# Performance work log

Hardware: AMD Instinct MI355X
Metric: run time of the kernel (lower is better)

## Reference

```python
import jax, jax.numpy as jnp
import numpy as np
from jax import lax

BS, T, D = 32, 2048, 256
H, L = 256, 2

def setup_inputs() -> dict:
    key = jax.random.key(0)
    ks = jax.random.split(key, 5)
    s = 1.0 / np.sqrt(H)
    x = jax.random.normal(ks[0], (BS, T, D), dtype=jnp.float32)
    Wx = jax.random.uniform(ks[1], (L, 3 * H, D), jnp.float32, -s, s)
    Wh = jax.random.uniform(ks[2], (L, 3 * H, H), jnp.float32, -s, s)
    bx = jax.random.uniform(ks[3], (L, 3 * H), jnp.float32, -s, s)
    bh = jax.random.uniform(ks[4], (L, 3 * H), jnp.float32, -s, s)
    return {"x": x, "Wx": Wx, "Wh": Wh, "bx": bx, "bh": bh}

def _gru_scan(gx, Wh, bh, h0):
    # gx: (T, bs, L, 3H) precomputed input-side gates; h0: (bs, L, H)
    def step(h, gx_t):
        gh = jnp.einsum('blh,lgh->blg', h, Wh) + bh  # (bs, L, 3H)
        xr, xz, xn = jnp.split(gx_t, 3, axis=-1)
        hr, hz, hn = jnp.split(gh, 3, axis=-1)
        r = jax.nn.sigmoid(xr + hr)
        z = jax.nn.sigmoid(xz + hz)
        n = jnp.tanh(xn + r * hn)
        h_new = (1.0 - z) * n + z * h
        return h_new, h_new
    _, hs = lax.scan(step, h0, gx)  # (T, bs, L, H)
    return hs

def reference(x, Wx, Wh, bx, bh):
    bs, t, _ = x.shape
    l, h = Wh.shape[0], Wh.shape[2]
    # Input-side gate projections for all timesteps/layers at once (each layer
    # consumes the raw input x_t, as in the source module).
    gx = jnp.einsum('btd,lgd->tblg', x, Wx) + bx  # (T, bs, L, 3H)
    h0 = jnp.zeros((bs, l, h), x.dtype)
    fwd = _gru_scan(gx, Wh, bh, h0)               # (T, bs, L, H)
    bwd = _gru_scan(gx[::-1], Wh, bh, h0)[::-1]   # reversed-time pass, same weights
    out = jnp.concatenate([fwd, bwd], axis=-1)    # (T, bs, L, 2H)
    # ordering matches source: for t in range(T): for layer in range(L)
    out = out.transpose(1, 0, 2, 3).reshape(bs, t * l, 2 * h)
    return out
```

## Files before the change

kernel.cpp:

```cpp
#include <hip/hip_runtime.h>


typedef _Float16 half8 __attribute__((ext_vector_type(8)));
typedef _Float16 half2_t __attribute__((ext_vector_type(2)));
typedef float floatx4 __attribute__((ext_vector_type(4)));

__device__ __forceinline__ float sigmoidf_fast(float x) {
    return 1.0f / (1.0f + __expf(-x));
}

__device__ __forceinline__ float tanh_fast(float x) {
    float ax = fabsf(x);
    float e = __expf(-2.0f * ax);
    float t = (1.0f - e) / (1.0f + e);
    return copysignf(t, x);
}

__global__ __launch_bounds__(256) void gemm_gx_kernel(
    const float* __restrict__ x,
    const float* __restrict__ Wx,
    const float* __restrict__ bx,
    _Float16* __restrict__ gx)
{
    __shared__ __align__(16) char lds[32768];
    _Float16* As = (_Float16*)lds;
    _Float16* Bs = (_Float16*)(lds + 8192);

    const int tid = threadIdx.x;
    const int m0 = blockIdx.x * 128;
    const int n0 = blockIdx.y * 128;
    const int wave = tid >> 6;
    const int lane = tid & 63;
    const int wm = wave & 1;
    const int wn = wave >> 1;
    const int frag = lane & 15;
    const int kg = lane >> 4;

    floatx4 acc[4][4];
#pragma unroll
    for (int a = 0; a < 4; ++a)
#pragma unroll
        for (int b = 0; b < 4; ++b)
            acc[a][b] = (floatx4){0.f, 0.f, 0.f, 0.f};

    for (int k0 = 0; k0 < 256; k0 += 32) {
        __syncthreads();
#pragma unroll
        for (int rep = 0; rep < 2; ++rep) {
            int idx = tid + rep * 256;
            int row = idx >> 2;
            int kc = idx & 3;
            const float4* ap = (const float4*)(x + (size_t)(m0 + row) * 256 + k0 + kc * 8);
            const float4* bp = (const float4*)(Wx + (size_t)(n0 + row) * 256 + k0 + kc * 8);
            float4 a0 = ap[0], a1 = ap[1];
            float4 b0 = bp[0], b1 = bp[1];
            half8 av = {(_Float16)a0.x, (_Float16)a0.y, (_Float16)a0.z, (_Float16)a0.w,
                        (_Float16)a1.x, (_Float16)a1.y, (_Float16)a1.z, (_Float16)a1.w};
            half8 bv = {(_Float16)b0.x, (_Float16)b0.y, (_Float16)b0.z, (_Float16)b0.w,
                        (_Float16)b1.x, (_Float16)b1.y, (_Float16)b1.z, (_Float16)b1.w};
            *(half8*)(As + (kc * 128 + row) * 8) = av;
            *(half8*)(Bs + (kc * 128 + row) * 8) = bv;
        }
        __syncthreads();

        half8 af[4], bfr[4];
#pragma unroll
        for (int tm = 0; tm < 4; ++tm)
            af[tm] = *(const half8*)(As + (kg * 128 + wm * 64 + tm * 16 + frag) * 8);
#pragma unroll
        for (int tn = 0; tn < 4; ++tn)
            bfr[tn] = *(const half8*)(Bs + (kg * 128 + wn * 64 + tn * 16 + frag) * 8);
#pragma unroll
        for (int tm = 0; tm < 4; ++tm)
#pragma unroll
            for (int tn = 0; tn < 4; ++tn)
                acc[tm][tn] = __builtin_amdgcn_mfma_f32_16x16x32_f16(
                    af[tm], bfr[tn], acc[tm][tn], 0, 0, 0);
    }

    __syncthreads();
    _Float16* epi = (_Float16*)lds;
#pragma unroll
    for (int tm = 0; tm < 4; ++tm) {
#pragma unroll
        for (int tn = 0; tn < 4; ++tn) {
            int col = wn * 64 + tn * 16 + frag;
            float bias = bx[n0 + col];
#pragma unroll
            for (int r = 0; r < 4; ++r) {
                int rowc = wm * 64 + tm * 16 + kg * 4 + r;
                epi[rowc * 128 + col] = (_Float16)(acc[tm][tn][r] + bias);
            }
        }
    }
    __syncthreads();

    int row = tid >> 1;
    int hs = tid & 1;
    int gm = m0 + row;
    int bb = gm >> 11;
    int tt = gm & 2047;
    int l = n0 / 768;
    int g0 = n0 - l * 768 + hs * 64;
    size_t oidx = (((size_t)bb * 2 + l) * 2048 + tt) * 768 + g0;
    const uint4* s = (const uint4*)(epi + row * 128 + hs * 64);
    uint4* d = (uint4*)(gx + oidx);
#pragma unroll
    for (int j = 0; j < 8; ++j) d[j] = s[j];
}

__global__ __launch_bounds__(512)
__attribute__((amdgpu_waves_per_eu(2, 2)))
void gru_scan_kernel(
    const float* __restrict__ Wh,
    const float* __restrict__ bh,
    const _Float16* __restrict__ gx,
    float* __restrict__ out)
{
    const int c = blockIdx.x;
    const int b = c & 31;
    const int l = (c >> 5) & 1;
    const int dir = c >> 6;
    const int tid = threadIdx.x;
    const int wave = tid >> 6;
    const int lane = tid & 63;
    const int q = lane >> 5;
    const int i = wave * 32 + (lane & 31);

    __shared__ __align__(16) _Float16 h2[2][256];

    half2_t wr[64], wz[64], wn_[64];
    {
        const float2* pr = (const float2*)(Wh + ((size_t)l * 768 + i) * 256 + q * 128);
        const float2* pz = (const float2*)(Wh + ((size_t)l * 768 + 256 + i) * 256 + q * 128);
        const float2* pn = (const float2*)(Wh + ((size_t)l * 768 + 512 + i) * 256 + q * 128);
#pragma unroll
        for (int j = 0; j < 64; ++j) {
            float2 a = pr[j], bb2 = pz[j], cc = pn[j];
            wr[j]  = (half2_t){(_Float16)a.x, (_Float16)a.y};
            wz[j]  = (half2_t){(_Float16)bb2.x, (_Float16)bb2.y};
            wn_[j] = (half2_t){(_Float16)cc.x, (_Float16)cc.y};
        }
    }

    const float bhr = bh[l * 768 + i];
    const float bhz = bh[l * 768 + 256 + i];
    const float bhn = bh[l * 768 + 512 + i];

    const _Float16* gxp = gx + (size_t)(b * 2 + l) * 2048 * 768;
    float* outp = out + (size_t)b * 2048 * 1024 + (size_t)l * 512 + dir * 256 + i;

    if (tid < 256) h2[0][tid] = (_Float16)0.f;

    const int t0 = dir ? 2047 : 0;
    _Float16 cxr = gxp[(size_t)t0 * 768 + i];
    _Float16 cxz = gxp[(size_t)t0 * 768 + 256 + i];
    _Float16 cxn = gxp[(size_t)t0 * 768 + 512 + i];
    __syncthreads();

    float hreg = 0.f;

    for (int s = 0; s < 2048; ++s) {
        const int t = dir ? (2047 - s) : s;
        const int sn = (s < 2047) ? (s + 1) : s;
        const int tn = dir ? (2047 - sn) : sn;

        _Float16 pxr = gxp[(size_t)tn * 768 + i];
        _Float16 pxz = gxp[(size_t)tn * 768 + 256 + i];
        _Float16 pxn = gxp[(size_t)tn * 768 + 512 + i];

        float ar = 0.f, az = 0.f, an = 0.f;
        const uint4* hbase = (const uint4*)(&h2[s & 1][0]) + (q << 4);
#pragma unroll
        for (int j = 0; j < 16; ++j) {
            uint4 hv = hbase[j];
            half2_t h0 = __builtin_bit_cast(half2_t, hv.x);
            half2_t h1 = __builtin_bit_cast(half2_t, hv.y);
            half2_t hg = __builtin_bit_cast(half2_t, hv.z);
            half2_t h3 = __builtin_bit_cast(half2_t, hv.w);
            ar = __builtin_amdgcn_fdot2(wr[4 * j + 0], h0, ar, false);
            az = __builtin_amdgcn_fdot2(wz[4 * j + 0], h0, az, false);
            an = __builtin_amdgcn_fdot2(wn_[4 * j + 0], h0, an, false);
            ar = __builtin_amdgcn_fdot2(wr[4 * j + 1], h1, ar, false);
            az = __builtin_amdgcn_fdot2(wz[4 * j + 1], h1, az, false);
            an = __builtin_amdgcn_fdot2(wn_[4 * j + 1], h1, an, false);
            ar = __builtin_amdgcn_fdot2(wr[4 * j + 2], hg, ar, false);
            az = __builtin_amdgcn_fdot2(wz[4 * j + 2], hg, az, false);
            an = __builtin_amdgcn_fdot2(wn_[4 * j + 2], hg, an, false);
            ar = __builtin_amdgcn_fdot2(wr[4 * j + 3], h3, ar, false);
            az = __builtin_amdgcn_fdot2(wz[4 * j + 3], h3, az, false);
            an = __builtin_amdgcn_fdot2(wn_[4 * j + 3], h3, an, false);
        }

        ar += __shfl_xor(ar, 32, 64);
        az += __shfl_xor(az, 32, 64);
        an += __shfl_xor(an, 32, 64);

        float r = sigmoidf_fast((float)cxr + ar + bhr);
        float z = sigmoidf_fast((float)cxz + az + bhz);
        float n = tanh_fast((float)cxn + an + r * (an * 0.f + (az * 0.f) + (ar * 0.f) + bhn + an - an + (float)0) + 0.f * an);
        (void)n;
        float ghn = an + bhn;
        n = tanh_fast((float)cxn + r * ghn);
        float hnew = (1.f - z) * n + z * hreg;
        hreg = hnew;

        if (q == 0) {
            outp[(size_t)t * 1024] = hnew;
            h2[(s + 1) & 1][i] = (_Float16)hnew;
        }
        cxr = pxr; cxz = pxz; cxn = pxn;
        __syncthreads();
    }
}

extern "C" void kernel_launch(void* const* d_in, const int* in_sizes, int n_in,
                              void* d_out, int out_size, void* d_ws, size_t ws_size,
                              hipStream_t stream) {
    const float* x  = (const float*)d_in[0];
    const float* Wx = (const float*)d_in[1];
    const float* Wh = (const float*)d_in[2];
    const float* bx = (const float*)d_in[3];
    const float* bh = (const float*)d_in[4];
    float* out = (float*)d_out;
    _Float16* gxbuf = (_Float16*)d_ws;

    gemm_gx_kernel<<<dim3(512, 12), 256, 0, stream>>>(x, Wx, bx, gxbuf);

    gru_scan_kernel<<<dim3(128), 512, 0, stream>>>(Wh, bh, gxbuf, out);
}
```

Before: 2.881 ms.

## Split GRU scan dot products across four lanes per unit with 1024 threads

The recurrent scan kernel now uses 1024 threads per block, so each hidden unit's 256-long dot product is split across four lane groups of 64 elements instead of two of 128. This halves per-thread weight registers and per-step serial FMA work, at the cost of an extra cross-lane shuffle reduction and a wider block barrier each step. The LDS reads of h are rotated per lane group to avoid bank conflicts, the dead redundant tanh computation is removed, and gx values are converted to float when loaded.

```diff
diff --git a/kernel.cpp b/kernel.cpp
--- a/kernel.cpp
+++ b/kernel.cpp
@@ -109,9 +109,7 @@
     for (int j = 0; j < 8; ++j) d[j] = s[j];
 }
 
-__global__ __launch_bounds__(512)
-__attribute__((amdgpu_waves_per_eu(2, 2)))
-void gru_scan_kernel(
+__global__ __launch_bounds__(1024) void gru_scan_kernel(
     const float* __restrict__ Wh,
     const float* __restrict__ bh,
     const _Float16* __restrict__ gx,
@@ -124,22 +122,28 @@
     const int tid = threadIdx.x;
     const int wave = tid >> 6;
     const int lane = tid & 63;
-    const int q = lane >> 5;
-    const int i = wave * 32 + (lane & 31);
+    const int q = lane >> 4;
+    const int i = wave * 16 + (lane & 15);
 
     __shared__ __align__(16) _Float16 h2[2][256];
 
-    half2_t wr[64], wz[64], wn_[64];
+    half2_t wr[32], wz[32], wn_[32];
     {
-        const float2* pr = (const float2*)(Wh + ((size_t)l * 768 + i) * 256 + q * 128);
-        const float2* pz = (const float2*)(Wh + ((size_t)l * 768 + 256 + i) * 256 + q * 128);
-        const float2* pn = (const float2*)(Wh + ((size_t)l * 768 + 512 + i) * 256 + q * 128);
-#pragma unroll
-        for (int j = 0; j < 64; ++j) {
-            float2 a = pr[j], bb2 = pz[j], cc = pn[j];
-            wr[j]  = (half2_t){(_Float16)a.x, (_Float16)a.y};
-            wz[j]  = (half2_t){(_Float16)bb2.x, (_Float16)bb2.y};
-            wn_[j] = (half2_t){(_Float16)cc.x, (_Float16)cc.y};
+        const float2* pr = (const float2*)(Wh + ((size_t)l * 768 + i) * 256 + q * 64);
+        const float2* pz = (const float2*)(Wh + ((size_t)l * 768 + 256 + i) * 256 + q * 64);
+        const float2* pn = (const float2*)(Wh + ((size_t)l * 768 + 512 + i) * 256 + q * 64);
+#pragma unroll
+        for (int j = 0; j < 8; ++j) {
+            int g = (j + 2 * q) & 7;
+#pragma unroll
+            for (int d = 0; d < 4; ++d) {
+                float2 a = pr[4 * g + d];
+                float2 bb2 = pz[4 * g + d];
+                float2 cc = pn[4 * g + d];
+                wr[4 * j + d]  = (half2_t){(_Float16)a.x, (_Float16)a.y};
+                wz[4 * j + d]  = (half2_t){(_Float16)bb2.x, (_Float16)bb2.y};
+                wn_[4 * j + d] = (half2_t){(_Float16)cc.x, (_Float16)cc.y};
+            }
         }
     }
 
@@ -153,9 +157,9 @@
     if (tid < 256) h2[0][tid] = (_Float16)0.f;
 
     const int t0 = dir ? 2047 : 0;
-    _Float16 cxr = gxp[(size_t)t0 * 768 + i];
-    _Float16 cxz = gxp[(size_t)t0 * 768 + 256 + i];
-    _Float16 cxn = gxp[(size_t)t0 * 768 + 512 + i];
+    float cxr = (float)gxp[(size_t)t0 * 768 + i];
+    float cxz = (float)gxp[(size_t)t0 * 768 + 256 + i];
+    float cxn = (float)gxp[(size_t)t0 * 768 + 512 + i];
     __syncthreads();
 
     float hreg = 0.f;
@@ -165,15 +169,15 @@
         const int sn = (s < 2047) ? (s + 1) : s;
         const int tn = dir ? (2047 - sn) : sn;
 
-        _Float16 pxr = gxp[(size_t)tn * 768 + i];
-        _Float16 pxz = gxp[(size_t)tn * 768 + 256 + i];
-        _Float16 pxn = gxp[(size_t)tn * 768 + 512 + i];
+        float pxr = (float)gxp[(size_t)tn * 768 + i];
+        float pxz = (float)gxp[(size_t)tn * 768 + 256 + i];
+        float pxn = (float)gxp[(size_t)tn * 768 + 512 + i];
 
         float ar = 0.f, az = 0.f, an = 0.f;
-        const uint4* hbase = (const uint4*)(&h2[s & 1][0]) + (q << 4);
-#pragma unroll
-        for (int j = 0; j < 16; ++j) {
-            uint4 hv = hbase[j];
+        const char* hb = (const char*)(&h2[s & 1][0]);
+#pragma unroll
+        for (int j = 0; j < 8; ++j) {
+            uint4 hv = *(const uint4*)(hb + q * 128 + (((j + 2 * q) & 7) << 4));
             half2_t h0 = __builtin_bit_cast(half2_t, hv.x);
             half2_t h1 = __builtin_bit_cast(half2_t, hv.y);
             half2_t hg = __builtin_bit_cast(half2_t, hv.z);
@@ -192,16 +196,16 @@
             an = __builtin_amdgcn_fdot2(wn_[4 * j + 3], h3, an, false);
         }
 
+        ar += __shfl_xor(ar, 16, 64);
         ar += __shfl_xor(ar, 32, 64);
+        az += __shfl_xor(az, 16, 64);
         az += __shfl_xor(az, 32, 64);
+        an += __shfl_xor(an, 16, 64);
         an += __shfl_xor(an, 32, 64);
 
-        float r = sigmoidf_fast((float)cxr + ar + bhr);
-        float z = sigmoidf_fast((float)cxz + az + bhz);
-        float n = tanh_fast((float)cxn + an + r * (an * 0.f + (az * 0.f) + (ar * 0.f) + bhn + an - an + (float)0) + 0.f * an);
-        (void)n;
-        float ghn = an + bhn;
-        n = tanh_fast((float)cxn + r * ghn);
+        float r = sigmoidf_fast(cxr + ar + bhr);
+        float z = sigmoidf_fast(cxz + az + bhz);
+        float n = tanh_fast(cxn + r * (an + bhn));
         float hnew = (1.f - z) * n + z * hreg;
         hreg = hnew;
 
@@ -227,5 +231,5 @@
 
     gemm_gx_kernel<<<dim3(512, 12), 256, 0, stream>>>(x, Wx, bx, gxbuf);
 
-    gru_scan_kernel<<<dim3(128), 512, 0, stream>>>(Wh, bh, gxbuf, out);
-}
+    gru_scan_kernel<<<dim3(128), 1024, 0, stream>>>(Wh, bh, gxbuf, out);
+}
```

New measurement: 3.802 ms. 32.0% more time.
